# Performance work log

Hardware: AMD Instinct MI355X
Metric: run time of the kernel (lower is better)

The kernel has to match this reference:

```python
import jax, jax.numpy as jnp
import numpy as np

D = 1024
B, LQ, LK = 8, 2048, 2048
NEG = -1e9


def setup_inputs() -> dict:
    key = jax.random.key(0)
    ks = jax.random.split(key, 8)
    query = jax.random.normal(ks[0], (B, LQ, D), dtype=jnp.float32)
    k_in = jax.random.normal(ks[1], (B, LK, D), dtype=jnp.float32)
    value = jax.random.normal(ks[2], (B, LK, D), dtype=jnp.float32)
    mask = jax.random.randint(ks[3], (B, LK), 0, 2, dtype=jnp.int32)
    s = 1.0 / np.sqrt(D)
    Wq_w = jax.random.normal(ks[4], (D, D), dtype=jnp.float32) * s
    Wq_b = jnp.zeros((D,), dtype=jnp.float32)
    Wk_w = jax.random.normal(ks[5], (D, D), dtype=jnp.float32) * s
    Wk_b = jnp.zeros((D,), dtype=jnp.float32)
    return {"query": query, "key": k_in, "value": value, "mask": mask,
            "Wq_w": Wq_w, "Wq_b": Wq_b, "Wk_w": Wk_w, "Wk_b": Wk_b}


def reference(query, key, value, mask, Wq_w, Wq_b, Wk_w, Wk_b):
    # Linear projections (torch Linear: x @ W.T + b)
    q = jnp.einsum('bld,ed->ble', query, Wq_w) + Wq_b  # [B, Lq, D]
    k = jnp.einsum('bld,ed->ble', key, Wk_w) + Wk_b    # [B, Lk, D]
    scale = 1.0 / jnp.sqrt(jnp.asarray(D, dtype=q.dtype))
    aw = jnp.einsum('bqd,bkd->bqk', q, k) * scale      # [B, Lq, Lk]
    # custom multiplicative + additive masking: mask -> [B, 1, Lk]
    m = mask.astype(aw.dtype)[:, None, :]
    aw = aw * m
    aw = jnp.where(m == 0, jnp.asarray(NEG, dtype=aw.dtype), aw)
    attn = jax.nn.softmax(aw, axis=-1)
    return jnp.einsum('bqk,bkd->bqd', attn, value)     # [B, Lq, D]
```

## Files before the change

kernel.cpp:

```cpp
#include <hip/hip_runtime.h>

typedef __bf16 bf16;
typedef __bf16 bf16x8 __attribute__((ext_vector_type(8)));
typedef __bf16 bf16x4 __attribute__((ext_vector_type(4)));
typedef float f32x4 __attribute__((ext_vector_type(4)));

__device__ __forceinline__ void gl_lds16(const bf16* g, bf16* l) {
  __builtin_amdgcn_global_load_lds(
      (__attribute__((address_space(1))) void*)g,
      (__attribute__((address_space(3))) void*)l, 16, 0, 0);
}

__global__ __launch_bounds__(256) void cvt_f32_bf16(
    const float* __restrict__ src, bf16* __restrict__ dst, int n8) {
  int i = blockIdx.x * 256 + threadIdx.x;
  if (i >= n8) return;
  const float4* s4 = (const float4*)src;
  float4 a = s4[2 * i], b = s4[2 * i + 1];
  bf16x8 o = {(bf16)a.x, (bf16)a.y, (bf16)a.z, (bf16)a.w,
              (bf16)b.x, (bf16)b.y, (bf16)b.z, (bf16)b.w};
  *(bf16x8*)(dst + (size_t)i * 8) = o;
}

__global__ __launch_bounds__(256) void transpose_v(
    const float* __restrict__ V, bf16* __restrict__ VT) {
  int b = blockIdx.z;
  const float* Vb = V + (size_t)b * 2048 * 1024;
  bf16* Tb = VT + (size_t)b * 1024 * 2048;
  __shared__ float tile[32][33];
  int tx = threadIdx.x, ty = threadIdx.y;
  int x = blockIdx.x * 32 + tx;
  int yb = blockIdx.y * 32;
#pragma unroll
  for (int j = 0; j < 4; j++)
    tile[ty + j * 8][tx] = Vb[(size_t)(yb + ty + j * 8) * 1024 + x];
  __syncthreads();
  int xo = yb + tx;
#pragma unroll
  for (int j = 0; j < 4; j++)
    Tb[(size_t)(blockIdx.x * 32 + ty + j * 8) * 2048 + xo] =
        (bf16)tile[tx][ty + j * 8];
}

template <int MODE>
__global__ __launch_bounds__(256) void gemm_bt(
    const bf16* __restrict__ A, const bf16* __restrict__ Bm,
    void* __restrict__ Cv, const float* __restrict__ bias,
    const int* __restrict__ mask, int M, int N, int K,
    long long sA, long long sB, long long sC) {
  const int b = blockIdx.z;
  const bf16* Ab = A + (long long)b * sA;
  const bf16* Bb = Bm + (long long)b * sB;
  const int m0 = blockIdx.y * 128, n0 = blockIdx.x * 128;
  __shared__ __align__(16) bf16 lA[128 * 64];
  __shared__ __align__(16) bf16 lB[128 * 64];
  const int tid = threadIdx.x, w = tid >> 6, lane = tid & 63;
  const int wm = (w >> 1) * 64, wn = (w & 1) * 64;
  const int lrow = lane >> 3;
  const int gsw = (((lane & 7) ^ lrow) * 8);

  f32x4 zero = {0.f, 0.f, 0.f, 0.f};
  f32x4 acc[4][4];
#pragma unroll
  for (int i = 0; i < 4; i++)
#pragma unroll
    for (int j = 0; j < 4; j++) acc[i][j] = zero;

  const bf16* Aq = Ab + (long long)m0 * K;
  const bf16* Bq = Bb + (long long)n0 * K;
  const int fr = lane & 15;
  const int fg = lane >> 4;
  const int frx = fr & 7;

  for (int ks = 0; ks < K; ks += 64) {
#pragma unroll
    for (int i = 0; i < 4; i++) {
      int t = w * 4 + i;
      int r = t * 8 + lrow;
      gl_lds16(Aq + (long long)r * K + (ks + gsw), &lA[t * 512]);
      gl_lds16(Bq + (long long)r * K + (ks + gsw), &lB[t * 512]);
    }
    __syncthreads();
#pragma unroll
    for (int kc = 0; kc < 2; kc++) {
      const int col = ((kc * 4 + fg) ^ frx) * 8;
      bf16x8 af[4], bfr[4];
#pragma unroll
      for (int mi = 0; mi < 4; mi++)
        af[mi] = *(const bf16x8*)&lA[(wm + mi * 16 + fr) * 64 + col];
#pragma unroll
      for (int ni = 0; ni < 4; ni++)
        bfr[ni] = *(const bf16x8*)&lB[(wn + ni * 16 + fr) * 64 + col];
#pragma unroll
      for (int mi = 0; mi < 4; mi++)
#pragma unroll
        for (int ni = 0; ni < 4; ni++)
          acc[mi][ni] = __builtin_amdgcn_mfma_f32_16x16x32_bf16(
              af[mi], bfr[ni], acc[mi][ni], 0, 0, 0);
    }
    __syncthreads();
  }

  const int erow = (lane >> 4) * 4, ecol = lane & 15;
  if constexpr (MODE == 0) {
    bf16* C = (bf16*)Cv;
#pragma unroll
    for (int mi = 0; mi < 4; mi++)
#pragma unroll
      for (int r = 0; r < 4; r++) {
        int row = m0 + wm + mi * 16 + erow + r;
#pragma unroll
        for (int ni = 0; ni < 4; ni++) {
          int col = n0 + wn + ni * 16 + ecol;
          C[(long long)row * N + col] = (bf16)(acc[mi][ni][r] + bias[col]);
        }
      }
  } else if constexpr (MODE == 1) {
    float* C = (float*)Cv + (long long)b * sC;
    const int* mb = mask + b * 2048;
#pragma unroll
    for (int ni = 0; ni < 4; ni++) {
      int col = n0 + wn + ni * 16 + ecol;
      bool keep = mb[col] != 0;
#pragma unroll
      for (int mi = 0; mi < 4; mi++)
#pragma unroll
        for (int r = 0; r < 4; r++) {
          int row = m0 + wm + mi * 16 + erow + r;
          C[(long long)row * N + col] = keep ? acc[mi][ni][r] * 0.03125f : -1e9f;
        }
    }
  } else {
    float* C = (float*)Cv + (long long)b * sC;
#pragma unroll
    for (int mi = 0; mi < 4; mi++)
#pragma unroll
      for (int r = 0; r < 4; r++) {
        int row = m0 + wm + mi * 16 + erow + r;
#pragma unroll
        for (int ni = 0; ni < 4; ni++) {
          int col = n0 + wn + ni * 16 + ecol;
          C[(long long)row * N + col] = acc[mi][ni][r];
        }
      }
  }
}

__global__ __launch_bounds__(256) void softmax_rows(
    const float* __restrict__ S, bf16* __restrict__ P) {
  long long row = blockIdx.x;
  const float4* src = (const float4*)(S + row * 2048);
  int tid = threadIdx.x, w = tid >> 6, lane = tid & 63;
  float4 v0 = src[tid], v1 = src[tid + 256];
  float m = fmaxf(fmaxf(fmaxf(v0.x, v0.y), fmaxf(v0.z, v0.w)),
                  fmaxf(fmaxf(v1.x, v1.y), fmaxf(v1.z, v1.w)));
#pragma unroll
  for (int off = 32; off; off >>= 1) m = fmaxf(m, __shfl_xor(m, off, 64));
  __shared__ float redm[4], reds[4];
  if (lane == 0) redm[w] = m;
  __syncthreads();
  m = fmaxf(fmaxf(redm[0], redm[1]), fmaxf(redm[2], redm[3]));
  float e[8];
  e[0] = __expf(v0.x - m); e[1] = __expf(v0.y - m);
  e[2] = __expf(v0.z - m); e[3] = __expf(v0.w - m);
  e[4] = __expf(v1.x - m); e[5] = __expf(v1.y - m);
  e[6] = __expf(v1.z - m); e[7] = __expf(v1.w - m);
  float s = e[0] + e[1] + e[2] + e[3] + e[4] + e[5] + e[6] + e[7];
#pragma unroll
  for (int off = 32; off; off >>= 1) s += __shfl_xor(s, off, 64);
  if (lane == 0) reds[w] = s;
  __syncthreads();
  s = reds[0] + reds[1] + reds[2] + reds[3];
  float inv = 1.0f / s;
  bf16x4 o0 = {(bf16)(e[0] * inv), (bf16)(e[1] * inv),
               (bf16)(e[2] * inv), (bf16)(e[3] * inv)};
  bf16x4 o1 = {(bf16)(e[4] * inv), (bf16)(e[5] * inv),
               (bf16)(e[6] * inv), (bf16)(e[7] * inv)};
  bf16* Pr = P + row * 2048;
  *(bf16x4*)(Pr + tid * 4) = o0;
  *(bf16x4*)(Pr + 1024 + tid * 4) = o1;
}

extern "C" void kernel_launch(void* const* d_in, const int* in_sizes, int n_in,
                              void* d_out, int out_size, void* d_ws,
                              size_t ws_size, hipStream_t stream) {
  const float* query = (const float*)d_in[0];
  const float* key_in = (const float*)d_in[1];
  const float* value = (const float*)d_in[2];
  const int* mask = (const int*)d_in[3];
  const float* Wq_w = (const float*)d_in[4];
  const float* Wq_b = (const float*)d_in[5];
  const float* Wk_w = (const float*)d_in[6];
  const float* Wk_b = (const float*)d_in[7];
  float* out = (float*)d_out;

  const size_t MB = 1ull << 20;
  char* base = (char*)d_ws;
  bf16* qx = (bf16*)(base + 0 * MB);
  bf16* kx = (bf16*)(base + 32 * MB);
  bf16* wq = (bf16*)(base + 64 * MB);
  bf16* wk = (bf16*)(base + 66 * MB);
  float* S = (float*)(base + 0 * MB);
  bf16* qp = (bf16*)(base + 128 * MB);
  bf16* kp = (bf16*)(base + 160 * MB);
  bf16* P = (bf16*)(base + 128 * MB);
  bf16* vt = (bf16*)(base + 192 * MB);

  cvt_f32_bf16<<<8192, 256, 0, stream>>>(query, qx, 2097152);
  cvt_f32_bf16<<<8192, 256, 0, stream>>>(key_in, kx, 2097152);
  cvt_f32_bf16<<<512, 256, 0, stream>>>(Wq_w, wq, 131072);
  cvt_f32_bf16<<<512, 256, 0, stream>>>(Wk_w, wk, 131072);
  transpose_v<<<dim3(32, 64, 8), dim3(32, 8), 0, stream>>>(value, vt);

  gemm_bt<0><<<dim3(8, 128, 1), 256, 0, stream>>>(
      qx, wq, qp, Wq_b, nullptr, 16384, 1024, 1024, 0, 0, 0);
  gemm_bt<0><<<dim3(8, 128, 1), 256, 0, stream>>>(
      kx, wk, kp, Wk_b, nullptr, 16384, 1024, 1024, 0, 0, 0);
  gemm_bt<1><<<dim3(16, 16, 8), 256, 0, stream>>>(
      qp, kp, S, nullptr, mask, 2048, 2048, 1024, 2048LL * 1024,
      2048LL * 1024, 2048LL * 2048);
  softmax_rows<<<16384, 256, 0, stream>>>(S, P);
  gemm_bt<2><<<dim3(8, 16, 8), 256, 0, stream>>>(
      P, vt, out, nullptr, nullptr, 2048, 1024, 2048, 2048LL * 2048,
      1024LL * 2048, 2048LL * 1024);
}
```

Baseline: 584.3 us.

## Switch GEMMs to 32x32x16 MFMA tiles and store attention scores as bf16

Replaces the 16x16x32 MFMA with 32x32x16 bf16 MFMA in all three GEMMs, which reduces LDS fragment loads per MFMA, and rewrites the epilogue indexing to match. The score matrix S is now written in bf16 instead of fp32, halving its write and softmax read traffic. The softmax kernel is rewritten to load and store 8 bf16 values per thread. Rounding the scores to bf16 before softmax reduces precision, although -1e9 stays representable.

New measurement: 556.5 us. -4.8%, faster.

```diff
diff --git a/kernel.cpp b/kernel.cpp
--- a/kernel.cpp
+++ b/kernel.cpp
@@ -2,8 +2,8 @@
 
 typedef __bf16 bf16;
 typedef __bf16 bf16x8 __attribute__((ext_vector_type(8)));
-typedef __bf16 bf16x4 __attribute__((ext_vector_type(4)));
 typedef float f32x4 __attribute__((ext_vector_type(4)));
+typedef float f32x16 __attribute__((ext_vector_type(16)));
 
 __device__ __forceinline__ void gl_lds16(const bf16* g, bf16* l) {
   __builtin_amdgcn_global_load_lds(
@@ -59,18 +59,19 @@
   const int lrow = lane >> 3;
   const int gsw = (((lane & 7) ^ lrow) * 8);
 
-  f32x4 zero = {0.f, 0.f, 0.f, 0.f};
-  f32x4 acc[4][4];
-#pragma unroll
-  for (int i = 0; i < 4; i++)
-#pragma unroll
-    for (int j = 0; j < 4; j++) acc[i][j] = zero;
+  f32x16 acc[2][2];
+#pragma unroll
+  for (int i = 0; i < 2; i++)
+#pragma unroll
+    for (int j = 0; j < 2; j++)
+#pragma unroll
+      for (int r = 0; r < 16; r++) acc[i][j][r] = 0.f;
 
   const bf16* Aq = Ab + (long long)m0 * K;
   const bf16* Bq = Bb + (long long)n0 * K;
-  const int fr = lane & 15;
-  const int fg = lane >> 4;
-  const int frx = fr & 7;
+  const int fr = lane & 31;
+  const int fh = lane >> 5;
+  const int key = lane & 7;
 
   for (int ks = 0; ks < K; ks += 64) {
 #pragma unroll
@@ -82,103 +83,106 @@
     }
     __syncthreads();
 #pragma unroll
-    for (int kc = 0; kc < 2; kc++) {
-      const int col = ((kc * 4 + fg) ^ frx) * 8;
-      bf16x8 af[4], bfr[4];
-#pragma unroll
-      for (int mi = 0; mi < 4; mi++)
-        af[mi] = *(const bf16x8*)&lA[(wm + mi * 16 + fr) * 64 + col];
-#pragma unroll
-      for (int ni = 0; ni < 4; ni++)
-        bfr[ni] = *(const bf16x8*)&lB[(wn + ni * 16 + fr) * 64 + col];
-#pragma unroll
-      for (int mi = 0; mi < 4; mi++)
-#pragma unroll
-        for (int ni = 0; ni < 4; ni++)
-          acc[mi][ni] = __builtin_amdgcn_mfma_f32_16x16x32_bf16(
+    for (int kc = 0; kc < 4; kc++) {
+      const int g = ((kc * 2 + fh) ^ key) * 8;
+      bf16x8 af[2], bfr[2];
+#pragma unroll
+      for (int mi = 0; mi < 2; mi++)
+        af[mi] = *(const bf16x8*)&lA[(wm + mi * 32 + fr) * 64 + g];
+#pragma unroll
+      for (int ni = 0; ni < 2; ni++)
+        bfr[ni] = *(const bf16x8*)&lB[(wn + ni * 32 + fr) * 64 + g];
+#pragma unroll
+      for (int mi = 0; mi < 2; mi++)
+#pragma unroll
+        for (int ni = 0; ni < 2; ni++)
+          acc[mi][ni] = __builtin_amdgcn_mfma_f32_32x32x16_bf16(
               af[mi], bfr[ni], acc[mi][ni], 0, 0, 0);
     }
     __syncthreads();
   }
 
-  const int erow = (lane >> 4) * 4, ecol = lane & 15;
+  const int ecol = lane & 31, er4 = (lane >> 5) * 4;
   if constexpr (MODE == 0) {
     bf16* C = (bf16*)Cv;
 #pragma unroll
-    for (int mi = 0; mi < 4; mi++)
-#pragma unroll
-      for (int r = 0; r < 4; r++) {
-        int row = m0 + wm + mi * 16 + erow + r;
-#pragma unroll
-        for (int ni = 0; ni < 4; ni++) {
-          int col = n0 + wn + ni * 16 + ecol;
-          C[(long long)row * N + col] = (bf16)(acc[mi][ni][r] + bias[col]);
+    for (int ni = 0; ni < 2; ni++) {
+      int col = n0 + wn + ni * 32 + ecol;
+      float bv = bias[col];
+#pragma unroll
+      for (int mi = 0; mi < 2; mi++)
+#pragma unroll
+        for (int r = 0; r < 16; r++) {
+          int row = m0 + wm + mi * 32 + er4 + (r & 3) + 8 * (r >> 2);
+          C[(long long)row * N + col] = (bf16)(acc[mi][ni][r] + bv);
         }
-      }
+    }
   } else if constexpr (MODE == 1) {
-    float* C = (float*)Cv + (long long)b * sC;
+    bf16* C = (bf16*)Cv + (long long)b * sC;
     const int* mb = mask + b * 2048;
 #pragma unroll
-    for (int ni = 0; ni < 4; ni++) {
-      int col = n0 + wn + ni * 16 + ecol;
+    for (int ni = 0; ni < 2; ni++) {
+      int col = n0 + wn + ni * 32 + ecol;
       bool keep = mb[col] != 0;
 #pragma unroll
-      for (int mi = 0; mi < 4; mi++)
-#pragma unroll
-        for (int r = 0; r < 4; r++) {
-          int row = m0 + wm + mi * 16 + erow + r;
-          C[(long long)row * N + col] = keep ? acc[mi][ni][r] * 0.03125f : -1e9f;
+      for (int mi = 0; mi < 2; mi++)
+#pragma unroll
+        for (int r = 0; r < 16; r++) {
+          int row = m0 + wm + mi * 32 + er4 + (r & 3) + 8 * (r >> 2);
+          C[(long long)row * N + col] =
+              keep ? (bf16)(acc[mi][ni][r] * 0.03125f) : (bf16)(-1e9f);
         }
     }
   } else {
     float* C = (float*)Cv + (long long)b * sC;
 #pragma unroll
-    for (int mi = 0; mi < 4; mi++)
-#pragma unroll
-      for (int r = 0; r < 4; r++) {
-        int row = m0 + wm + mi * 16 + erow + r;
-#pragma unroll
-        for (int ni = 0; ni < 4; ni++) {
-          int col = n0 + wn + ni * 16 + ecol;
+    for (int ni = 0; ni < 2; ni++) {
+      int col = n0 + wn + ni * 32 + ecol;
+#pragma unroll
+      for (int mi = 0; mi < 2; mi++)
+#pragma unroll
+        for (int r = 0; r < 16; r++) {
+          int row = m0 + wm + mi * 32 + er4 + (r & 3) + 8 * (r >> 2);
           C[(long long)row * N + col] = acc[mi][ni][r];
         }
-      }
+    }
   }
 }
 
 __global__ __launch_bounds__(256) void softmax_rows(
-    const float* __restrict__ S, bf16* __restrict__ P) {
+    const bf16* __restrict__ S, bf16* __restrict__ P) {
   long long row = blockIdx.x;
-  const float4* src = (const float4*)(S + row * 2048);
+  const bf16x8* src = (const bf16x8*)(S + row * 2048);
   int tid = threadIdx.x, w = tid >> 6, lane = tid & 63;
-  float4 v0 = src[tid], v1 = src[tid + 256];
-  float m = fmaxf(fmaxf(fmaxf(v0.x, v0.y), fmaxf(v0.z, v0.w)),
-                  fmaxf(fmaxf(v1.x, v1.y), fmaxf(v1.z, v1.w)));
+  bf16x8 v = src[tid];
+  float f[8];
+#pragma unroll
+  for (int i = 0; i < 8; i++) f[i] = (float)v[i];
+  float m = f[0];
+#pragma unroll
+  for (int i = 1; i < 8; i++) m = fmaxf(m, f[i]);
 #pragma unroll
   for (int off = 32; off; off >>= 1) m = fmaxf(m, __shfl_xor(m, off, 64));
   __shared__ float redm[4], reds[4];
   if (lane == 0) redm[w] = m;
   __syncthreads();
   m = fmaxf(fmaxf(redm[0], redm[1]), fmaxf(redm[2], redm[3]));
-  float e[8];
-  e[0] = __expf(v0.x - m); e[1] = __expf(v0.y - m);
-  e[2] = __expf(v0.z - m); e[3] = __expf(v0.w - m);
-  e[4] = __expf(v1.x - m); e[5] = __expf(v1.y - m);
-  e[6] = __expf(v1.z - m); e[7] = __expf(v1.w - m);
-  float s = e[0] + e[1] + e[2] + e[3] + e[4] + e[5] + e[6] + e[7];
+  float e[8], s = 0.f;
+#pragma unroll
+  for (int i = 0; i < 8; i++) {
+    e[i] = __expf(f[i] - m);
+    s += e[i];
+  }
 #pragma unroll
   for (int off = 32; off; off >>= 1) s += __shfl_xor(s, off, 64);
   if (lane == 0) reds[w] = s;
   __syncthreads();
   s = reds[0] + reds[1] + reds[2] + reds[3];
   float inv = 1.0f / s;
-  bf16x4 o0 = {(bf16)(e[0] * inv), (bf16)(e[1] * inv),
-               (bf16)(e[2] * inv), (bf16)(e[3] * inv)};
-  bf16x4 o1 = {(bf16)(e[4] * inv), (bf16)(e[5] * inv),
-               (bf16)(e[6] * inv), (bf16)(e[7] * inv)};
-  bf16* Pr = P + row * 2048;
-  *(bf16x4*)(Pr + tid * 4) = o0;
-  *(bf16x4*)(Pr + 1024 + tid * 4) = o1;
+  bf16x8 o;
+#pragma unroll
+  for (int i = 0; i < 8; i++) o[i] = (bf16)(e[i] * inv);
+  *(bf16x8*)(P + row * 2048 + tid * 8) = o;
 }
 
 extern "C" void kernel_launch(void* const* d_in, const int* in_sizes, int n_in,
@@ -200,7 +204,7 @@
   bf16* kx = (bf16*)(base + 32 * MB);
   bf16* wq = (bf16*)(base + 64 * MB);
   bf16* wk = (bf16*)(base + 66 * MB);
-  float* S = (float*)(base + 0 * MB);
+  bf16* S = (bf16*)(base + 0 * MB);
   bf16* qp = (bf16*)(base + 128 * MB);
   bf16* kp = (bf16*)(base + 160 * MB);
   bf16* P = (bf16*)(base + 128 * MB);
```
